# Kernel optimization log

Measured on AMD Instinct MI355X. Metric: run time of the kernel, lower is better.

Reference implementation:

```python
import jax, jax.numpy as jnp
import numpy as np

B, L, H, E = 32, 256, 8, 16
SEQ_LEN = 64          # init seq_len, used only in final view
OUT = 256             # out_channels, must be divisible by SEQ_LEN
A = E + 1 + 128       # augmented channels: original + time + conv(128)
SIG_CH = A + A * A    # depth-2 signature channels
DN = ('NWC', 'WIO', 'NWC')


def setup_inputs() -> dict:
    key = jax.random.key(0)
    ks = jax.random.split(key, 8)
    return {
        'q': jax.random.normal(ks[0], (B, L, H, E), jnp.float32),
        'k': jax.random.normal(ks[1], (B, L, H, E), jnp.float32),
        'v': jax.random.normal(ks[2], (B, L, H, E), jnp.float32),
        'mask': jnp.zeros((B, L), jnp.bool_),
        'conv1_w': jax.random.normal(ks[3], (3, E, 64), jnp.float32) * 0.1,
        'conv1_b': jnp.zeros((64,), jnp.float32),
        'conv2_w': jax.random.normal(ks[4], (1, 64, 128), jnp.float32) * 0.1,
        'conv2_b': jnp.zeros((128,), jnp.float32),
        'lin_w': jax.random.normal(ks[5], (SIG_CH, OUT), jnp.float32) * 0.01,
        'lin_b': jnp.zeros((OUT,), jnp.float32),
    }


def _signature_depth2(p):
    # p: [N, S, C] piecewise-linear path. Returns [N, C + C*C].
    dx = p[:, 1:] - p[:, :-1]                       # [N, S-1, C]
    s1 = dx.sum(axis=1)                             # level 1
    cum_excl = jnp.cumsum(dx, axis=1) - dx          # sum of increments before t
    # level 2: sum_{s<t} dx_s (x) dx_t + 0.5 * dx_t (x) dx_t
    s2 = jnp.einsum('nti,ntj->nij', cum_excl + 0.5 * dx, dx)
    return jnp.concatenate([s1, s2.reshape(s2.shape[0], -1)], axis=-1)


def reference(q, k, v, mask, conv1_w, conv1_b, conv2_w, conv2_b, lin_w, lin_b):
    Bq, Lq, Hq, Eq = q.shape
    x = q.transpose(0, 2, 1, 3).reshape(Bq * Hq, Lq, Eq)   # [N, L, E]
    T = Lq - 3 + 1                                          # valid-conv length, kernel 3
    # Augment pieces
    trunc = x[:, 2:]                                        # [N, T, E]
    time = jnp.broadcast_to(jnp.linspace(0.0, 1.0, T, dtype=x.dtype)[None, :, None],
                            (Bq * Hq, T, 1))
    a = jax.lax.conv_general_dilated(x, conv1_w, (1,), 'VALID', dimension_numbers=DN) + conv1_b
    a = jax.nn.relu(jax.lax.conv_general_dilated(a, conv2_w, (1,), 'VALID', dimension_numbers=DN) + conv2_b)
    aug = jnp.concatenate([trunc, time, a], axis=2)         # [N, T, A]
    # lead-lag transform as written in source: interleave along time -> [N, 2T, A]
    lag = jnp.concatenate([aug[:, 1:], aug[:, -1:]], axis=1)
    ll = jnp.stack([aug, lag], axis=2).reshape(aug.shape[0], 2 * T, aug.shape[2])
    sig = _signature_depth2(ll)                             # [N, SIG_CH]
    out = sig @ lin_w + lin_b                               # [N, OUT]
    return out.reshape(Bq, Hq, SEQ_LEN, -1)
```

## Files before the change

### kernel.cpp

```cpp
#include <hip/hip_runtime.h>
#include <hip/hip_bf16.h>

#define Bq 32
#define Lq 256
#define Hq 8
#define Eq 16
#define Nn (Bq*Hq)
#define T 254
#define A 145
#define SIG_CH (A + A*A)
#define KP 21184
#define OUT 256

typedef __attribute__((ext_vector_type(8))) short short8;
typedef __attribute__((ext_vector_type(8))) unsigned short ushort8;
typedef __attribute__((ext_vector_type(4))) float floatx4;

static __device__ __forceinline__ unsigned short f2bf(float v) {
    unsigned int u = __float_as_uint(v);
    unsigned int r = (u + 0x7FFFu + ((u >> 16) & 1u)) >> 16;
    return (unsigned short)r;
}
static __device__ __forceinline__ float bf2f(unsigned short b) {
    return __uint_as_float(((unsigned int)b) << 16);
}

__global__ __launch_bounds__(256) void wprep_kernel(
    const float* __restrict__ W,
    unsigned short* __restrict__ wt_hi, unsigned short* __restrict__ wt_lo,
    const float* __restrict__ w1, const float* __restrict__ w2,
    unsigned short* __restrict__ w1im_hi, unsigned short* __restrict__ w1im_lo,
    unsigned short* __restrict__ w2t_hi,  unsigned short* __restrict__ w2t_lo,
    const float* __restrict__ lb, float* __restrict__ out)
{
    const int tid = threadIdx.x;
    const int bid = blockIdx.x;

    if (bid >= 1372) {
        out[(bid - 1372)*256 + tid] = lb[tid];
        return;
    }
    if (bid >= 1324) {
        int idx = (bid - 1324)*256 + tid;
        if (idx < 4096) {
            int c = idx & 63, k = idx >> 6;
            float v = (k < 48) ? w1[k*64 + c] : 0.f;
            unsigned short hb = f2bf(v);
            w1im_hi[c*64 + k] = hb;
            w1im_lo[c*64 + k] = f2bf(v - bf2f(hb));
        } else {
            int j = idx - 4096;
            int c = j & 127, i = j >> 7;
            float v = w2[i*128 + c];
            unsigned short hb = f2bf(v);
            w2t_hi[c*64 + i] = hb;
            w2t_lo[c*64 + i] = f2bf(v - bf2f(hb));
        }
        return;
    }

    __shared__ float ls[64][65];
    const int k0 = (bid % 331) * 64;
    const int o0 = (bid / 331) * 64;

    #pragma unroll
    for (int p = 0; p < 16; ++p) {
        int idx = tid + p*256;
        int kk = idx >> 6, oo = idx & 63;
        int k = k0 + kk;
        ls[kk][oo] = (k < SIG_CH) ? W[(long)k*OUT + o0 + oo] : 0.f;
    }
    __syncthreads();

    const int ob = tid >> 3;
    const int kq = (tid & 7) * 8;
    #pragma unroll
    for (int p = 0; p < 2; ++p) {
        int o = p*32 + ob;
        unsigned short hbuf[8], lbuf[8];
        #pragma unroll
        for (int j = 0; j < 8; ++j) {
            float v = ls[kq + j][o];
            unsigned short hb = f2bf(v);
            hbuf[j] = hb;
            lbuf[j] = f2bf(v - bf2f(hb));
        }
        long off = (long)(o0 + o)*KP + k0 + kq;
        *(ushort8*)(wt_hi + off) = *(ushort8*)hbuf;
        *(ushort8*)(wt_lo + off) = *(ushort8*)lbuf;
    }
}

#define MDS 40
#define OS3 36
#define XIS 72

__global__ __launch_bounds__(256) void augsig_kernel(
    const float* __restrict__ q,
    const float* __restrict__ b1, const float* __restrict__ b2,
    const unsigned short* __restrict__ w1im_hi, const unsigned short* __restrict__ w1im_lo,
    const unsigned short* __restrict__ w2t_hi,  const unsigned short* __restrict__ w2t_lo,
    unsigned short* __restrict__ sig_hi, unsigned short* __restrict__ sig_lo)
{
    __shared__ __align__(16) unsigned short mdb[3*160*MDS];
    __shared__ __align__(16) float outs[A*OS3];
    __shared__ __align__(16) float xsc[36*16];
    __shared__ __align__(16) float b1s[64];
    __shared__ __align__(16) float b2s[128];

    unsigned short* Mh = mdb;
    unsigned short* Ml = mdb + 160*MDS;
    unsigned short* Dh = mdb + 2*160*MDS;
    unsigned short* ximh = mdb;
    unsigned short* ximl = mdb + 3456;
    unsigned short* a1h  = mdb + 6912;
    unsigned short* a1l  = mdb + 10368;

    const int tid = threadIdx.x;
    const int n = blockIdx.x;
    const int b = n >> 3, h = n & 7;

    const int lane = tid & 63;
    const int wv   = tid >> 6;
    const int frow = lane & 15;
    const int quad = lane >> 4;
    const int wm = wv & 1, wn = wv >> 1;

    if (tid < 64)  b1s[tid] = b1[tid];
    if (tid < 128) b2s[tid] = b2[tid];

    const float4* q4 = (const float4*)q + ((long)(b*Lq)*Hq + h)*4;
    const float inv253 = 1.0f / 253.0f;

    short8 c1bh[2], c1bl[2];
    #pragma unroll
    for (int ks = 0; ks < 2; ++ks) {
        int br = (wv*16 + frow)*64 + ks*32 + quad*8;
        c1bh[ks] = *(const short8*)(w1im_hi + br);
        c1bl[ks] = *(const short8*)(w1im_lo + br);
    }
    short8 c2bh[2][2], c2bl[2][2];
    #pragma unroll
    for (int nt = 0; nt < 2; ++nt)
        #pragma unroll
        for (int ks = 0; ks < 2; ++ks) {
            int br = (wv*32 + nt*16 + frow)*64 + ks*32 + quad*8;
            c2bh[nt][ks] = *(const short8*)(w2t_hi + br);
            c2bl[nt][ks] = *(const short8*)(w2t_lo + br);
        }

    float a0 = 0.f, vlast = 0.f;

    floatx4 acc[5][5];
    #pragma unroll
    for (int i = 0; i < 5; ++i)
        #pragma unroll
        for (int j = 0; j < 5; ++j)
            acc[i][j] = (floatx4){0.f, 0.f, 0.f, 0.f};

    if (tid < 140) {
        int r = tid >> 2, e4 = tid & 3;
        int t = r; if (t > 255) t = 255;
        *((float4*)xsc + (r*4 + e4)) = q4[t*32 + e4];
    }
    __syncthreads();

    #pragma unroll 1
    for (int c = 0; c < 8; ++c) {
        const int t0 = c*32;

        for (int idx = tid; idx < 48*8; idx += 256) {
            int r = idx >> 3, g = idx & 7;
            unsigned short hh[8], ll[8];
            if (r <= 32 && g < 6) {
                const float* src = &xsc[r*16 + g*8];
                #pragma unroll
                for (int e = 0; e < 8; ++e) {
                    float v = src[e];
                    unsigned short hbv = f2bf(v);
                    hh[e] = hbv; ll[e] = f2bf(v - bf2f(hbv));
                }
            } else {
                #pragma unroll
                for (int e = 0; e < 8; ++e) { hh[e] = 0; ll[e] = 0; }
            }
            *(ushort8*)&ximh[r*XIS + g*8] = *(ushort8*)hh;
            *(ushort8*)&ximl[r*XIS + g*8] = *(ushort8*)ll;
        }
        __syncthreads();

        {
            short8 ah[3][2], al[3][2];
            #pragma unroll
            for (int mt = 0; mt < 3; ++mt)
                #pragma unroll
                for (int ks = 0; ks < 2; ++ks) {
                    int ar = (mt*16 + frow)*XIS + ks*32 + quad*8;
                    ah[mt][ks] = *(const short8*)&ximh[ar];
                    al[mt][ks] = *(const short8*)&ximl[ar];
                }
            floatx4 acc1[3];
            #pragma unroll
            for (int mt = 0; mt < 3; ++mt) acc1[mt] = (floatx4){0.f,0.f,0.f,0.f};
            #pragma unroll
            for (int mt = 0; mt < 3; ++mt)
                #pragma unroll
                for (int ks = 0; ks < 2; ++ks) {
                    acc1[mt] = __builtin_amdgcn_mfma_f32_16x16x32_bf16(ah[mt][ks], c1bh[ks], acc1[mt], 0,0,0);
                    acc1[mt] = __builtin_amdgcn_mfma_f32_16x16x32_bf16(ah[mt][ks], c1bl[ks], acc1[mt], 0,0,0);
                    acc1[mt] = __builtin_amdgcn_mfma_f32_16x16x32_bf16(al[mt][ks], c1bh[ks], acc1[mt], 0,0,0);
                }
            const int cc = wv*16 + frow;
            const float bias = b1s[cc];
            #pragma unroll
            for (int mt = 0; mt < 3; ++mt)
                #pragma unroll
                for (int e = 0; e < 4; ++e) {
                    int t = mt*16 + quad*4 + e;
                    float v = acc1[mt][e] + bias;
                    unsigned short hbv = f2bf(v);
                    a1h[t*XIS + cc] = hbv;
                    a1l[t*XIS + cc] = f2bf(v - bf2f(hbv));
                }
        }
        __syncthreads();

        {
            short8 ah[3][2], al[3][2];
            #pragma unroll
            for (int mt = 0; mt < 3; ++mt)
                #pragma unroll
                for (int ks = 0; ks < 2; ++ks) {
                    int ar = (mt*16 + frow)*XIS + ks*32 + quad*8;
                    ah[mt][ks] = *(const short8*)&a1h[ar];
                    al[mt][ks] = *(const short8*)&a1l[ar];
                }
            floatx4 acc2[3][2];
            #pragma unroll
            for (int mt = 0; mt < 3; ++mt)
                #pragma unroll
                for (int nt = 0; nt < 2; ++nt)
                    acc2[mt][nt] = (floatx4){0.f,0.f,0.f,0.f};
            #pragma unroll
            for (int mt = 0; mt < 3; ++mt)
                #pragma unroll
                for (int nt = 0; nt < 2; ++nt)
                    #pragma unroll
                    for (int ks = 0; ks < 2; ++ks) {
                        acc2[mt][nt] = __builtin_amdgcn_mfma_f32_16x16x32_bf16(ah[mt][ks], c2bh[nt][ks], acc2[mt][nt], 0,0,0);
                        acc2[mt][nt] = __builtin_amdgcn_mfma_f32_16x16x32_bf16(ah[mt][ks], c2bl[nt][ks], acc2[mt][nt], 0,0,0);
                        acc2[mt][nt] = __builtin_amdgcn_mfma_f32_16x16x32_bf16(al[mt][ks], c2bh[nt][ks], acc2[mt][nt], 0,0,0);
                    }
            #pragma unroll
            for (int mt = 0; mt < 3; ++mt)
                #pragma unroll
                for (int nt = 0; nt < 2; ++nt) {
                    int cc = wv*32 + nt*16 + frow;
                    float bias = b2s[cc];
                    int tb = mt*16 + quad*4;
                    if (tb <= 32) {
                        float4 vv;
                        vv.x = fmaxf(acc2[mt][nt][0] + bias, 0.f);
                        vv.y = fmaxf(acc2[mt][nt][1] + bias, 0.f);
                        vv.z = fmaxf(acc2[mt][nt][2] + bias, 0.f);
                        vv.w = fmaxf(acc2[mt][nt][3] + bias, 0.f);
                        *(float4*)&outs[(17 + cc)*OS3 + tb] = vv;
                    }
                }
        }
        for (int idx = tid; idx < 17*33; idx += 256) {
            int ch = idx / 33, tt = idx - ch*33;
            float val = (ch < 16) ? xsc[(tt+2)*16 + ch] : (float)(t0+tt)*inv253;
            outs[ch*OS3 + tt] = val;
        }
        __syncthreads();

        if (tid < 160) {
            unsigned short mh[32], ml[32], dh[32];
            if (tid < A) {
                float v[33];
                #pragma unroll
                for (int i = 0; i < 8; ++i)
                    *(float4*)&v[i*4] = *(const float4*)&outs[tid*OS3 + i*4];
                v[32] = outs[tid*OS3 + 32];
                if (c == 0) a0 = v[0];
                if (c == 7) vlast = v[29];
                #pragma unroll
                for (int tl = 0; tl < 32; ++tl) {
                    bool valid = (t0 + tl) <= 252;
                    float x0 = v[tl], x1 = v[tl+1];
                    float d = valid ? (x1 - x0) : 0.f;
                    float m = valid ? (0.5f*(x0 + x1) - a0) : 0.f;
                    unsigned short hbv = f2bf(m);
                    mh[tl] = hbv; ml[tl] = f2bf(m - bf2f(hbv));
                    dh[tl] = f2bf(d);
                }
            } else {
                #pragma unroll
                for (int tl = 0; tl < 32; ++tl) { mh[tl]=0; ml[tl]=0; dh[tl]=0; }
            }
            #pragma unroll
            for (int pp = 0; pp < 4; ++pp) {
                *(ushort8*)&Mh[tid*MDS + pp*8] = *(ushort8*)&mh[pp*8];
                *(ushort8*)&Ml[tid*MDS + pp*8] = *(ushort8*)&ml[pp*8];
                *(ushort8*)&Dh[tid*MDS + pp*8] = *(ushort8*)&dh[pp*8];
            }
        } else if (c < 7) {
            for (int idx = tid - 160; idx < 140; idx += 96) {
                int r = idx >> 2, e4 = idx & 3;
                int t = (c+1)*32 + r; if (t > 255) t = 255;
                *((float4*)xsc + (r*4 + e4)) = q4[t*32 + e4];
            }
        }
        __syncthreads();

        {
            short8 afh[5], afl[5], bfh[5];
            #pragma unroll
            for (int i = 0; i < 5; ++i) {
                int ar = (wm*80 + i*16 + frow)*MDS + quad*8;
                int br = (wn*80 + i*16 + frow)*MDS + quad*8;
                afh[i] = *(const short8*)&Mh[ar];
                afl[i] = *(const short8*)&Ml[ar];
                bfh[i] = *(const short8*)&Dh[br];
            }
            #pragma unroll
            for (int mt = 0; mt < 5; ++mt)
                #pragma unroll
                for (int nt = 0; nt < 5; ++nt) {
                    acc[mt][nt] = __builtin_amdgcn_mfma_f32_16x16x32_bf16(
                        afh[mt], bfh[nt], acc[mt][nt], 0, 0, 0);
                    acc[mt][nt] = __builtin_amdgcn_mfma_f32_16x16x32_bf16(
                        afl[mt], bfh[nt], acc[mt][nt], 0, 0, 0);
                }
        }
        __syncthreads();
    }

    unsigned short* sh = sig_hi + (long)n*KP;
    unsigned short* sl = sig_lo + (long)n*KP;
    if (tid < A) {
        float v = vlast - a0;
        unsigned short hbv = f2bf(v);
        sh[tid] = hbv;
        sl[tid] = f2bf(v - bf2f(hbv));
    }
    if (tid >= 160 && tid < 160 + (KP - SIG_CH)) {
        sh[SIG_CH + tid - 160] = 0;
        sl[SIG_CH + tid - 160] = 0;
    }
    #pragma unroll
    for (int mt = 0; mt < 5; ++mt)
        #pragma unroll
        for (int nt = 0; nt < 5; ++nt) {
            int j = wn*80 + nt*16 + frow;
            int ib = wm*80 + mt*16 + quad*4;
            #pragma unroll
            for (int e = 0; e < 4; ++e) {
                int i = ib + e;
                if (i < A && j < A) {
                    float v = acc[mt][nt][e];
                    unsigned short hbv = f2bf(v);
                    sh[A + i*A + j] = hbv;
                    sl[A + i*A + j] = f2bf(v - bf2f(hbv));
                }
            }
        }
}

#define SPLITK 61
#define KC 352
#define NSTEP (KC/32)
#define LDA 40

__global__ __launch_bounds__(256) void gemm_kernel(
    const unsigned short* __restrict__ sig_hi, const unsigned short* __restrict__ sig_lo,
    const unsigned short* __restrict__ wt_hi,  const unsigned short* __restrict__ wt_lo,
    float* __restrict__ out)
{
    __shared__ __align__(16) unsigned short Ah[128*LDA];
    __shared__ __align__(16) unsigned short Al[128*LDA];
    __shared__ __align__(16) unsigned short Bh[64*LDA];
    __shared__ __align__(16) unsigned short Bl[64*LDA];

    const int tid = threadIdx.x;
    const int o0 = blockIdx.x * 64;
    const int n0 = blockIdx.y * 128;
    const int z  = blockIdx.z;
    const int k0 = z * KC;

    const int lane = tid & 63;
    const int w    = tid >> 6;
    const int wm   = w & 1;
    const int wn   = w >> 1;
    const int frow = lane & 15;
    const int quad = lane >> 4;

    const int srowA = tid >> 1;
    const int khA   = (tid & 1) * 16;
    const int srowB = tid >> 2;
    const int kqB   = (tid & 3) * 8;

    const unsigned short* gAh = sig_hi + (long)(n0 + srowA)*KP;
    const unsigned short* gAl = sig_lo + (long)(n0 + srowA)*KP;
    const unsigned short* gBh = wt_hi  + (long)(o0 + srowB)*KP;
    const unsigned short* gBl = wt_lo  + (long)(o0 + srowB)*KP;

    ushort8 rah[2], ral[2], rbh, rbl;
    const ushort8 z8 = {0,0,0,0,0,0,0,0};

    #define GLOAD(s)                                                          \
        {                                                                     \
            int kb = k0 + (s)*32;                                             \
            if (kb < KP) {                                                    \
                rah[0] = *(const ushort8*)(gAh + kb + khA);                   \
                rah[1] = *(const ushort8*)(gAh + kb + khA + 8);               \
                ral[0] = *(const ushort8*)(gAl + kb + khA);                   \
                ral[1] = *(const ushort8*)(gAl + kb + khA + 8);               \
                rbh    = *(const ushort8*)(gBh + kb + kqB);                   \
                rbl    = *(const ushort8*)(gBl + kb + kqB);                   \
            } else {                                                          \
                rah[0]=z8; rah[1]=z8; ral[0]=z8; ral[1]=z8;                   \
                rbh=z8; rbl=z8;                                               \
            }                                                                 \
        }

    #define LSTORE()                                                          \
        {                                                                     \
            int oA = srowA*LDA + khA;                                         \
            *(ushort8*)(Ah + oA)     = rah[0];                                \
            *(ushort8*)(Ah + oA + 8) = rah[1];                                \
            *(ushort8*)(Al + oA)     = ral[0];                                \
            *(ushort8*)(Al + oA + 8) = ral[1];                                \
            int oB = srowB*LDA + kqB;                                         \
            *(ushort8*)(Bh + oB) = rbh;                                       \
            *(ushort8*)(Bl + oB) = rbl;                                       \
        }

    floatx4 acc[4][2];
    #pragma unroll
    for (int i = 0; i < 4; ++i)
        #pragma unroll
        for (int j = 0; j < 2; ++j)
            acc[i][j] = (floatx4){0.f, 0.f, 0.f, 0.f};

    GLOAD(0);
    LSTORE();
    __syncthreads();

    for (int s = 0; s < NSTEP; ++s) {
        if (s < NSTEP-1) GLOAD(s+1);

        short8 afh[4], afl[4], bfh[2], bfl[2];
        const int aoff = (wm*64 + frow)*LDA + quad*8;
        const int boff = (wn*32 + frow)*LDA + quad*8;
        #pragma unroll
        for (int tI = 0; tI < 4; ++tI) {
            afh[tI] = *(const short8*)(Ah + aoff + tI*16*LDA);
            afl[tI] = *(const short8*)(Al + aoff + tI*16*LDA);
        }
        #pragma unroll
        for (int tI = 0; tI < 2; ++tI) {
            bfh[tI] = *(const short8*)(Bh + boff + tI*16*LDA);
            bfl[tI] = *(const short8*)(Bl + boff + tI*16*LDA);
        }
        #pragma unroll
        for (int mt = 0; mt < 4; ++mt)
            #pragma unroll
            for (int nt = 0; nt < 2; ++nt) {
                acc[mt][nt] = __builtin_amdgcn_mfma_f32_16x16x32_bf16(
                    afh[mt], bfh[nt], acc[mt][nt], 0, 0, 0);
                acc[mt][nt] = __builtin_amdgcn_mfma_f32_16x16x32_bf16(
                    afh[mt], bfl[nt], acc[mt][nt], 0, 0, 0);
                acc[mt][nt] = __builtin_amdgcn_mfma_f32_16x16x32_bf16(
                    afl[mt], bfh[nt], acc[mt][nt], 0, 0, 0);
            }
        __syncthreads();
        if (s < NSTEP-1) {
            LSTORE();
            __syncthreads();
        }
    }

    #pragma unroll
    for (int mt = 0; mt < 4; ++mt)
        #pragma unroll
        for (int nt = 0; nt < 2; ++nt) {
            int col = o0 + wn*32 + nt*16 + frow;
            int rbase = n0 + wm*64 + mt*16 + quad*4;
            #pragma unroll
            for (int e = 0; e < 4; ++e)
                atomicAdd(&out[(long)(rbase + e)*OUT + col], acc[mt][nt][e]);
        }
}

extern "C" void kernel_launch(void* const* d_in, const int* in_sizes, int n_in,
                              void* d_out, int out_size, void* d_ws, size_t ws_size,
                              hipStream_t stream) {
    const float* q  = (const float*)d_in[0];
    const float* w1 = (const float*)d_in[4];
    const float* b1 = (const float*)d_in[5];
    const float* w2 = (const float*)d_in[6];
    const float* b2 = (const float*)d_in[7];
    const float* lw = (const float*)d_in[8];
    const float* lb = (const float*)d_in[9];
    float* out = (float*)d_out;

    char* ws = (char*)d_ws;
    unsigned short* sig_hi  = (unsigned short*)ws;
    unsigned short* sig_lo  = (unsigned short*)(ws + 10846208);
    unsigned short* wt_hi   = (unsigned short*)(ws + 21692416);
    unsigned short* wt_lo   = (unsigned short*)(ws + 32538624);
    unsigned short* w1im_hi = (unsigned short*)(ws + 43384832);
    unsigned short* w1im_lo = (unsigned short*)(ws + 43384832 + 8192);
    unsigned short* w2t_hi  = (unsigned short*)(ws + 43384832 + 16384);
    unsigned short* w2t_lo  = (unsigned short*)(ws + 43384832 + 32768);

    wprep_kernel<<<1628, 256, 0, stream>>>(lw, wt_hi, wt_lo,
                                           w1, w2, w1im_hi, w1im_lo, w2t_hi, w2t_lo,
                                           lb, out);
    augsig_kernel<<<Nn, 256, 0, stream>>>(q, b1, b2, w1im_hi, w1im_lo, w2t_hi, w2t_lo, sig_hi, sig_lo);
    gemm_kernel<<<dim3(4, 2, SPLITK), 256, 0, stream>>>(sig_hi, sig_lo, wt_hi, wt_lo, out);
}
```

Baseline: 169.7 us.

## Fuse weight-prep and augment-signature kernels into one launch

Merges the weight conversion kernel and the augment/signature kernel into a single launch. Blocks 0-255 do the signature work, the next blocks transpose and split the linear weight into bf16 hi/lo, and the last blocks initialise the output with the bias. The conv weights are now converted to bf16 hi/lo in registers inside each signature block, removing the staging buffers. The q-tile prefetch that overlapped with the M/D build is replaced by a synchronous load at the start of each chunk. This saves a launch and lets the weight prep run alongside the signature work, at the cost of extra global reads per block and lost load/compute overlap.

```diff
diff --git a/kernel.cpp b/kernel.cpp
--- a/kernel.cpp
+++ b/kernel.cpp
@@ -25,88 +25,67 @@
     return __uint_as_float(((unsigned int)b) << 16);
 }
 
-__global__ __launch_bounds__(256) void wprep_kernel(
-    const float* __restrict__ W,
-    unsigned short* __restrict__ wt_hi, unsigned short* __restrict__ wt_lo,
-    const float* __restrict__ w1, const float* __restrict__ w2,
-    unsigned short* __restrict__ w1im_hi, unsigned short* __restrict__ w1im_lo,
-    unsigned short* __restrict__ w2t_hi,  unsigned short* __restrict__ w2t_lo,
-    const float* __restrict__ lb, float* __restrict__ out)
-{
-    const int tid = threadIdx.x;
-    const int bid = blockIdx.x;
-
-    if (bid >= 1372) {
-        out[(bid - 1372)*256 + tid] = lb[tid];
-        return;
-    }
-    if (bid >= 1324) {
-        int idx = (bid - 1324)*256 + tid;
-        if (idx < 4096) {
-            int c = idx & 63, k = idx >> 6;
-            float v = (k < 48) ? w1[k*64 + c] : 0.f;
-            unsigned short hb = f2bf(v);
-            w1im_hi[c*64 + k] = hb;
-            w1im_lo[c*64 + k] = f2bf(v - bf2f(hb));
-        } else {
-            int j = idx - 4096;
-            int c = j & 127, i = j >> 7;
-            float v = w2[i*128 + c];
-            unsigned short hb = f2bf(v);
-            w2t_hi[c*64 + i] = hb;
-            w2t_lo[c*64 + i] = f2bf(v - bf2f(hb));
-        }
-        return;
-    }
-
-    __shared__ float ls[64][65];
-    const int k0 = (bid % 331) * 64;
-    const int o0 = (bid / 331) * 64;
-
-    #pragma unroll
-    for (int p = 0; p < 16; ++p) {
-        int idx = tid + p*256;
-        int kk = idx >> 6, oo = idx & 63;
-        int k = k0 + kk;
-        ls[kk][oo] = (k < SIG_CH) ? W[(long)k*OUT + o0 + oo] : 0.f;
-    }
-    __syncthreads();
-
-    const int ob = tid >> 3;
-    const int kq = (tid & 7) * 8;
-    #pragma unroll
-    for (int p = 0; p < 2; ++p) {
-        int o = p*32 + ob;
-        unsigned short hbuf[8], lbuf[8];
-        #pragma unroll
-        for (int j = 0; j < 8; ++j) {
-            float v = ls[kq + j][o];
-            unsigned short hb = f2bf(v);
-            hbuf[j] = hb;
-            lbuf[j] = f2bf(v - bf2f(hb));
-        }
-        long off = (long)(o0 + o)*KP + k0 + kq;
-        *(ushort8*)(wt_hi + off) = *(ushort8*)hbuf;
-        *(ushort8*)(wt_lo + off) = *(ushort8*)lbuf;
-    }
-}
-
 #define MDS 40
 #define OS3 36
 #define XIS 72
 
-__global__ __launch_bounds__(256) void augsig_kernel(
+__global__ __launch_bounds__(256) void fused_kernel(
     const float* __restrict__ q,
-    const float* __restrict__ b1, const float* __restrict__ b2,
-    const unsigned short* __restrict__ w1im_hi, const unsigned short* __restrict__ w1im_lo,
-    const unsigned short* __restrict__ w2t_hi,  const unsigned short* __restrict__ w2t_lo,
-    unsigned short* __restrict__ sig_hi, unsigned short* __restrict__ sig_lo)
+    const float* __restrict__ w1, const float* __restrict__ b1,
+    const float* __restrict__ w2, const float* __restrict__ b2,
+    const float* __restrict__ W,  const float* __restrict__ lb,
+    unsigned short* __restrict__ sig_hi, unsigned short* __restrict__ sig_lo,
+    unsigned short* __restrict__ wt_hi,  unsigned short* __restrict__ wt_lo,
+    float* __restrict__ out)
 {
     __shared__ __align__(16) unsigned short mdb[3*160*MDS];
     __shared__ __align__(16) float outs[A*OS3];
     __shared__ __align__(16) float xsc[36*16];
     __shared__ __align__(16) float b1s[64];
     __shared__ __align__(16) float b2s[128];
+
+    const int tid = threadIdx.x;
+    const int bid = blockIdx.x;
+
+    if (bid >= 1580) {
+        out[(bid - 1580)*256 + tid] = lb[tid];
+        return;
+    }
+
+    if (bid >= 256) {
+        float* ls = (float*)mdb;
+        const int wid = bid - 256;
+        const int k0 = (wid % 331) * 64;
+        const int o0 = (wid / 331) * 64;
+
+        #pragma unroll
+        for (int p = 0; p < 16; ++p) {
+            int idx = tid + p*256;
+            int kk = idx >> 6, oo = idx & 63;
+            int k = k0 + kk;
+            ls[kk*65 + oo] = (k < SIG_CH) ? W[(long)k*OUT + o0 + oo] : 0.f;
+        }
+        __syncthreads();
+
+        const int ob = tid >> 3;
+        const int kq = (tid & 7) * 8;
+        #pragma unroll
+        for (int p = 0; p < 2; ++p) {
+            int o = p*32 + ob;
+            unsigned short hbuf[8], lbuf[8];
+            #pragma unroll
+            for (int j = 0; j < 8; ++j) {
+                float v = ls[(kq + j)*65 + o];
+                unsigned short hb = f2bf(v);
+                hbuf[j] = hb;
+                lbuf[j] = f2bf(v - bf2f(hb));
+            }
+            long off = (long)(o0 + o)*KP + k0 + kq;
+            *(ushort8*)(wt_hi + off) = *(ushort8*)hbuf;
+            *(ushort8*)(wt_lo + off) = *(ushort8*)lbuf;
+        }
+        return;
+    }
 
     unsigned short* Mh = mdb;
     unsigned short* Ml = mdb + 160*MDS;
@@ -116,8 +95,7 @@
     unsigned short* a1h  = mdb + 6912;
     unsigned short* a1l  = mdb + 10368;
 
-    const int tid = threadIdx.x;
-    const int n = blockIdx.x;
+    const int n = bid;
     const int b = n >> 3, h = n & 7;
 
     const int lane = tid & 63;
@@ -135,18 +113,34 @@
     short8 c1bh[2], c1bl[2];
     #pragma unroll
     for (int ks = 0; ks < 2; ++ks) {
-        int br = (wv*16 + frow)*64 + ks*32 + quad*8;
-        c1bh[ks] = *(const short8*)(w1im_hi + br);
-        c1bl[ks] = *(const short8*)(w1im_lo + br);
+        const int ccol = wv*16 + frow;
+        unsigned short hbuf[8], lbuf[8];
+        #pragma unroll
+        for (int e = 0; e < 8; ++e) {
+            int k = ks*32 + quad*8 + e;
+            float v = (k < 48) ? w1[k*64 + ccol] : 0.f;
+            unsigned short hb2 = f2bf(v);
+            hbuf[e] = hb2; lbuf[e] = f2bf(v - bf2f(hb2));
+        }
+        c1bh[ks] = *(short8*)hbuf;
+        c1bl[ks] = *(short8*)lbuf;
     }
     short8 c2bh[2][2], c2bl[2][2];
     #pragma unroll
     for (int nt = 0; nt < 2; ++nt)
         #pragma unroll
         for (int ks = 0; ks < 2; ++ks) {
-            int br = (wv*32 + nt*16 + frow)*64 + ks*32 + quad*8;
-            c2bh[nt][ks] = *(const short8*)(w2t_hi + br);
-            c2bl[nt][ks] = *(const short8*)(w2t_lo + br);
+            const int ccol = wv*32 + nt*16 + frow;
+            unsigned short hbuf[8], lbuf[8];
+            #pragma unroll
+            for (int e = 0; e < 8; ++e) {
+                int i = ks*32 + quad*8 + e;
+                float v = w2[i*128 + ccol];
+                unsigned short hb2 = f2bf(v);
+                hbuf[e] = hb2; lbuf[e] = f2bf(v - bf2f(hb2));
+            }
+            c2bh[nt][ks] = *(short8*)hbuf;
+            c2bl[nt][ks] = *(short8*)lbuf;
         }
 
     float a0 = 0.f, vlast = 0.f;
@@ -158,16 +152,16 @@
         for (int j = 0; j < 5; ++j)
             acc[i][j] = (floatx4){0.f, 0.f, 0.f, 0.f};
 
-    if (tid < 140) {
-        int r = tid >> 2, e4 = tid & 3;
-        int t = r; if (t > 255) t = 255;
-        *((float4*)xsc + (r*4 + e4)) = q4[t*32 + e4];
-    }
-    __syncthreads();
-
     #pragma unroll 1
     for (int c = 0; c < 8; ++c) {
         const int t0 = c*32;
+
+        if (tid < 140) {
+            int r = tid >> 2, e4 = tid & 3;
+            int t = t0 + r; if (t > 255) t = 255;
+            *((float4*)xsc + (r*4 + e4)) = q4[t*32 + e4];
+        }
+        __syncthreads();
 
         for (int idx = tid; idx < 48*8; idx += 256) {
             int r = idx >> 3, g = idx & 7;
@@ -304,12 +298,6 @@
                 *(ushort8*)&Mh[tid*MDS + pp*8] = *(ushort8*)&mh[pp*8];
                 *(ushort8*)&Ml[tid*MDS + pp*8] = *(ushort8*)&ml[pp*8];
                 *(ushort8*)&Dh[tid*MDS + pp*8] = *(ushort8*)&dh[pp*8];
-            }
-        } else if (c < 7) {
-            for (int idx = tid - 160; idx < 140; idx += 96) {
-                int r = idx >> 2, e4 = idx & 3;
-                int t = (c+1)*32 + r; if (t > 255) t = 255;
-                *((float4*)xsc + (r*4 + e4)) = q4[t*32 + e4];
             }
         }
         __syncthreads();
@@ -511,14 +499,8 @@
     unsigned short* sig_lo  = (unsigned short*)(ws + 10846208);
     unsigned short* wt_hi   = (unsigned short*)(ws + 21692416);
     unsigned short* wt_lo   = (unsigned short*)(ws + 32538624);
-    unsigned short* w1im_hi = (unsigned short*)(ws + 43384832);
-    unsigned short* w1im_lo = (unsigned short*)(ws + 43384832 + 8192);
-    unsigned short* w2t_hi  = (unsigned short*)(ws + 43384832 + 16384);
-    unsigned short* w2t_lo  = (unsigned short*)(ws + 43384832 + 32768);
-
-    wprep_kernel<<<1628, 256, 0, stream>>>(lw, wt_hi, wt_lo,
-                                           w1, w2, w1im_hi, w1im_lo, w2t_hi, w2t_lo,
-                                           lb, out);
-    augsig_kernel<<<Nn, 256, 0, stream>>>(q, b1, b2, w1im_hi, w1im_lo, w2t_hi, w2t_lo, sig_hi, sig_lo);
+
+    fused_kernel<<<1836, 256, 0, stream>>>(q, w1, b1, w2, b2, lw, lb,
+                                           sig_hi, sig_lo, wt_hi, wt_lo, out);
     gemm_kernel<<<dim3(4, 2, SPLITK), 256, 0, stream>>>(sig_hi, sig_lo, wt_hi, wt_lo, out);
 }
```

Result: slower. 174.6 us (+2.9%).
